# Kernel optimization log

Hardware: AMD Instinct MI355X
Metric: run time of the kernel (lower is better)

## Reference

```python
import jax, jax.numpy as jnp
import numpy as np

N_NODES = 100000
N_EDGES = 1250000
D = 64


def setup_inputs() -> dict:
    key = jax.random.key(0)
    k0, k1, k2, k3, k4 = jax.random.split(key, 5)
    feat = jax.random.normal(k0, (N_NODES, D), dtype=jnp.float32)
    src = jax.random.randint(k1, (N_EDGES,), 0, N_NODES)
    dst = jax.random.randint(k2, (N_EDGES,), 0, N_NODES)
    # GIN apply_func: Linear(D, D) -> ReLU -> Linear(D, D)
    scale = 1.0 / np.sqrt(D)
    W1 = jax.random.uniform(k3, (D, D), dtype=jnp.float32, minval=-scale, maxval=scale)
    b1 = jnp.zeros((D,), dtype=jnp.float32)
    W2 = jax.random.uniform(k4, (D, D), dtype=jnp.float32, minval=-scale, maxval=scale)
    b2 = jnp.zeros((D,), dtype=jnp.float32)
    eps = jnp.zeros((1,), dtype=jnp.float32)  # learnable eps, init 0
    return {"feat": feat, "W1": W1, "b1": b1, "W2": W2, "b2": b2,
            "eps": eps, "src": src, "dst": dst}


def reference(feat, W1, b1, W2, b2, eps, src, dst):
    # copy_u + sum reduce: gather source features per edge, scatter-add to dst
    msgs = feat[src]                                   # [E, D]
    neigh = jax.ops.segment_sum(msgs, dst, num_segments=feat.shape[0])  # [N, D]
    rst = (1.0 + eps) * feat + neigh                   # combine
    # apply_func (f_Theta): 2-layer MLP
    h = jax.nn.relu(rst @ W1 + b1)
    out = h @ W2 + b2
    return out
```

## Files before the change

kernel.cpp:

```cpp
#include <hip/hip_runtime.h>
#include <hip/hip_bf16.h>

#define N_NODES 100000
#define N_EDGES 1250000
#define DIM 64
#define NB 782
#define NCHUNK 512
#define CHUNK 2442
#define MAXE 4096

typedef __attribute__((ext_vector_type(8))) short short8;
typedef __attribute__((ext_vector_type(8))) __bf16 bf16x8;
typedef __attribute__((ext_vector_type(4))) float f32x4;

static __device__ __forceinline__ short f2bf(float f) {
    union { float f; unsigned u; } v; v.f = f;
    unsigned r = (v.u + 0x7fffu + ((v.u >> 16) & 1u)) >> 16;
    return (short)r;
}
static __device__ __forceinline__ float bflo(unsigned u) {
    union { unsigned u; float f; } v; v.u = u << 16; return v.f;
}
static __device__ __forceinline__ float bfhi(unsigned u) {
    union { unsigned u; float f; } v; v.u = u & 0xffff0000u; return v.f;
}
static __device__ __forceinline__ float bfs2f(short s) {
    union { unsigned u; float f; } v; v.u = ((unsigned)(unsigned short)s) << 16; return v.f;
}
static __device__ __forceinline__ int wave_scan(int v, int lane) {
#pragma unroll
    for (int off = 1; off < 64; off <<= 1) {
        int n = __shfl_up(v, off, 64);
        if (lane >= off) v += n;
    }
    return v;
}

__global__ __launch_bounds__(256) void prologue(const float* __restrict__ feat,
                                                short* __restrict__ featbf,
                                                const float* __restrict__ W1,
                                                const float* __restrict__ W2,
                                                short* __restrict__ wf,
                                                int basePrep) {
    int blk = blockIdx.x;
    if (blk < basePrep) {
        int i = (blk * 256 + threadIdx.x) * 8;
        float4 a = *(const float4*)(feat + i);
        float4 b = *(const float4*)(feat + i + 4);
        short8 t;
        t[0] = f2bf(a.x); t[1] = f2bf(a.y); t[2] = f2bf(a.z); t[3] = f2bf(a.w);
        t[4] = f2bf(b.x); t[5] = f2bf(b.y); t[6] = f2bf(b.z); t[7] = f2bf(b.w);
        *(short8*)(featbf + i) = t;
    } else {
        int idx = (blk - basePrep) * 256 + threadIdx.x;
        int layer = idx >> 12;
        int fi = idx & 4095;
        int fragidx = fi >> 9;
        int lane = (fi >> 3) & 63;
        int jj = fi & 7;
        int ct = fragidx >> 1, kt = fragidx & 1;
        int k = kt * 32 + (lane >> 4) * 8 + jj;
        int j = ct * 16 + (lane & 15);
        const float* W = layer ? W2 : W1;
        wf[idx] = f2bf(W[k * DIM + j]);
    }
}

__global__ __launch_bounds__(512) void partition3(const int* __restrict__ src,
                                                  const int* __restrict__ dst,
                                                  int* __restrict__ offs_gT,
                                                  int* __restrict__ edgebuf) {
    __shared__ int cnt[NB];
    __shared__ int lcur[NB];
    __shared__ int wsum[8];
    __shared__ int estage[CHUNK];

    int c = blockIdx.x;
    int t = threadIdx.x;
    int lane = t & 63, wv = t >> 6;
    int base = c * CHUNK;
    int end = base + CHUNK; if (end > N_EDGES) end = N_EDGES;

    for (int b = t; b < NB; b += 512) cnt[b] = 0;
    __syncthreads();
    for (int i = base + t; i < end; i += 512)
        atomicAdd(&cnt[dst[i] >> 7], 1);
    __syncthreads();

    int b0 = 2 * t, b1 = 2 * t + 1;
    int v0 = (b0 < NB) ? cnt[b0] : 0;
    int v1 = (b1 < NB) ? cnt[b1] : 0;
    int isc = wave_scan(v0 + v1, lane);
    if (lane == 63) wsum[wv] = isc;
    __syncthreads();
    if (wv == 0) {
        int s = (lane < 8) ? wsum[lane] : 0;
#pragma unroll
        for (int off = 1; off < 8; off <<= 1) {
            int n = __shfl_up(s, off, 64);
            if (lane >= off) s += n;
        }
        if (lane < 8) wsum[lane] = s;
    }
    __syncthreads();
    int ex = (wv ? wsum[wv - 1] : 0) + isc - (v0 + v1);
    if (b0 < NB) { lcur[b0] = ex;      offs_gT[(size_t)b0 * NCHUNK + c] = ex; }
    if (b1 < NB) { lcur[b1] = ex + v0; offs_gT[(size_t)b1 * NCHUNK + c] = ex + v0; }
    if (t == 511) offs_gT[(size_t)NB * NCHUNK + c] = wsum[7];
    __syncthreads();

    for (int i = base + t; i < end; i += 512) {
        int d = dst[i];
        int p = atomicAdd(&lcur[d >> 7], 1);
        estage[p] = src[i] | ((d & 127) << 17);
    }
    __syncthreads();

    int n = end - base;
    for (int i = t; i < n; i += 512) edgebuf[base + i] = estage[i];
}

template<int BF>
__global__ __launch_bounds__(512) void fused_gather_mlp(const int* __restrict__ offs_gT,
                                                        const int* __restrict__ edgebuf,
                                                        const void* __restrict__ featp,
                                                        const float* __restrict__ feat,
                                                        const short* __restrict__ wf,
                                                        const float* __restrict__ b1,
                                                        const float* __restrict__ b2,
                                                        const float* __restrict__ epsp,
                                                        float* __restrict__ out) {
    __shared__ union {
        struct { int ew[MAXE]; int es[MAXE]; } s;
        float tile[128][66];
    } u;
    __shared__ int cnt[128], offs[128], cur[128];
    __shared__ int slen[NCHUNK], dloc[NCHUNK];
    __shared__ int wsum[8];
    __shared__ int csum[2];

    int b = blockIdx.x;
    int node0 = b << 7;
    int tid = threadIdx.x;
    int lane = tid & 63, wv8 = tid >> 6;
    int c = tid & 15;
    int slot = tid >> 4;

    int s0 = offs_gT[(size_t)b * NCHUNK + tid];
    int myslen = offs_gT[(size_t)(b + 1) * NCHUNK + tid] - s0;
    int isc = wave_scan(myslen, lane);
    if (lane == 63) wsum[wv8] = isc;
    __syncthreads();
    if (wv8 == 0) {
        int s = (lane < 8) ? wsum[lane] : 0;
#pragma unroll
        for (int off = 1; off < 8; off <<= 1) {
            int n = __shfl_up(s, off, 64);
            if (lane >= off) s += n;
        }
        if (lane < 8) wsum[lane] = s;
    }
    __syncthreads();
    int incl = (wv8 ? wsum[wv8 - 1] : 0) + isc;
    dloc[tid] = incl - myslen;
    slen[tid] = myslen;
    int ec = wsum[7];
    __syncthreads();

    float acc[4][4];
#pragma unroll
    for (int g = 0; g < 4; ++g)
#pragma unroll
        for (int j = 0; j < 4; ++j) acc[g][j] = 0.f;

    int c0 = 0;
    while (c0 < NCHUNK) {
        int rbase = dloc[c0];
        int pred = (tid >= c0) && (dloc[tid] + slen[tid] - rbase <= MAXE);
        int nc = __syncthreads_count(pred);
        int c1 = c0 + nc;

        if (tid < 128) cnt[tid] = 0;
        if (tid >= c0 && tid < c1 && myslen > 0) {
            int d0 = dloc[tid] - rbase;
            const int* sp = edgebuf + (size_t)tid * CHUNK + s0;
            for (int i = 0; i < myslen; ++i) u.s.ew[d0 + i] = sp[i];
        }
        __syncthreads();

        int n = ((c1 < NCHUNK) ? dloc[c1] : ec) - rbase;

        for (int i = tid; i < n; i += 512)
            atomicAdd(&cnt[(u.s.ew[i] >> 17) & 127], 1);
        __syncthreads();

        int v_c = (tid < 128) ? cnt[tid] : 0;
        int s_c = 0;
        if (wv8 < 2) {
            s_c = wave_scan(v_c, lane);
            if (lane == 63) csum[wv8] = s_c;
        }
        __syncthreads();
        if (tid < 128) {
            int basec = (wv8 == 1) ? csum[0] : 0;
            int x = basec + s_c - v_c;
            offs[tid] = x;
            cur[tid] = x;
        }
        __syncthreads();

        for (int i = tid; i < n; i += 512) {
            int w = u.s.ew[i];
            int p = atomicAdd(&cur[(w >> 17) & 127], 1);
            u.s.es[p] = w & 0x1FFFF;
        }
        __syncthreads();

#pragma unroll
        for (int g = 0; g < 4; ++g) {
            int ld = g * 32 + slot;
            int e0 = offs[ld], e1 = e0 + cnt[ld];
            int i = e0;
            if (BF) {
                const uint2* fb = (const uint2*)featp;
                int nfull = (e1 - e0) & ~3;
                int efull = e0 + nfull;
                if (nfull) {
                    uint2 p0 = fb[u.s.es[i]     * 16 + c];
                    uint2 p1 = fb[u.s.es[i + 1] * 16 + c];
                    uint2 p2 = fb[u.s.es[i + 2] * 16 + c];
                    uint2 p3 = fb[u.s.es[i + 3] * 16 + c];
                    for (i = e0 + 4; i < efull; i += 4) {
                        uint2 q0 = fb[u.s.es[i]     * 16 + c];
                        uint2 q1 = fb[u.s.es[i + 1] * 16 + c];
                        uint2 q2 = fb[u.s.es[i + 2] * 16 + c];
                        uint2 q3 = fb[u.s.es[i + 3] * 16 + c];
                        acc[g][0] += bflo(p0.x) + bflo(p1.x) + bflo(p2.x) + bflo(p3.x);
                        acc[g][1] += bfhi(p0.x) + bfhi(p1.x) + bfhi(p2.x) + bfhi(p3.x);
                        acc[g][2] += bflo(p0.y) + bflo(p1.y) + bflo(p2.y) + bflo(p3.y);
                        acc[g][3] += bfhi(p0.y) + bfhi(p1.y) + bfhi(p2.y) + bfhi(p3.y);
                        p0 = q0; p1 = q1; p2 = q2; p3 = q3;
                    }
                    acc[g][0] += bflo(p0.x) + bflo(p1.x) + bflo(p2.x) + bflo(p3.x);
                    acc[g][1] += bfhi(p0.x) + bfhi(p1.x) + bfhi(p2.x) + bfhi(p3.x);
                    acc[g][2] += bflo(p0.y) + bflo(p1.y) + bflo(p2.y) + bflo(p3.y);
                    acc[g][3] += bfhi(p0.y) + bfhi(p1.y) + bfhi(p2.y) + bfhi(p3.y);
                }
                for (; i < e1; ++i) {
                    uint2 pa = fb[u.s.es[i] * 16 + c];
                    acc[g][0] += bflo(pa.x); acc[g][1] += bfhi(pa.x);
                    acc[g][2] += bflo(pa.y); acc[g][3] += bfhi(pa.y);
                }
            } else {
                const float4* ff = (const float4*)featp;
                int nfull = (e1 - e0) & ~1;
                int efull = e0 + nfull;
                if (nfull) {
                    float4 p0 = ff[u.s.es[i]     * 16 + c];
                    float4 p1 = ff[u.s.es[i + 1] * 16 + c];
                    for (i = e0 + 2; i < efull; i += 2) {
                        float4 q0 = ff[u.s.es[i]     * 16 + c];
                        float4 q1 = ff[u.s.es[i + 1] * 16 + c];
                        acc[g][0] += p0.x + p1.x; acc[g][1] += p0.y + p1.y;
                        acc[g][2] += p0.z + p1.z; acc[g][3] += p0.w + p1.w;
                        p0 = q0; p1 = q1;
                    }
                    acc[g][0] += p0.x + p1.x; acc[g][1] += p0.y + p1.y;
                    acc[g][2] += p0.z + p1.z; acc[g][3] += p0.w + p1.w;
                }
                for (; i < e1; ++i) {
                    float4 qa = ff[u.s.es[i] * 16 + c];
                    acc[g][0] += qa.x; acc[g][1] += qa.y;
                    acc[g][2] += qa.z; acc[g][3] += qa.w;
                }
            }
        }
        __syncthreads();
        c0 = c1;
    }

#pragma unroll
    for (int g = 0; g < 4; ++g) {
        int ld = g * 32 + slot;
#pragma unroll
        for (int j = 0; j < 4; ++j)
            u.tile[ld][c * 4 + j] = acc[g][j];
    }
    __syncthreads();

    int r = lane & 15, gg = lane >> 4;
    int lrow = wv8 * 16 + r;
    int node = node0 + lrow;
    bool valid = node < N_NODES;
    float epsv = 1.0f + epsp[0];

    const short8* w1f8 = (const short8*)(wf);
    const short8* w2f8 = (const short8*)(wf + 4096);

    short8 a[2];
#pragma unroll
    for (int kt = 0; kt < 2; ++kt) {
        float fv[8];
        if (BF) {
            short8 f8 = { 0,0,0,0,0,0,0,0 };
            if (valid) f8 = ((const short8*)featp)[node * 8 + kt * 4 + gg];
#pragma unroll
            for (int jj = 0; jj < 8; ++jj) fv[jj] = bfs2f(f8[jj]);
        } else {
            float4 f0 = { 0,0,0,0 }, f1 = { 0,0,0,0 };
            if (valid) {
                const float* fp = feat + (size_t)node * 64 + kt * 32 + gg * 8;
                f0 = *(const float4*)fp;
                f1 = *(const float4*)(fp + 4);
            }
            fv[0]=f0.x; fv[1]=f0.y; fv[2]=f0.z; fv[3]=f0.w;
            fv[4]=f1.x; fv[5]=f1.y; fv[6]=f1.z; fv[7]=f1.w;
        }
        const float2* tp = (const float2*)&u.tile[lrow][kt * 32 + gg * 8];
        float2 n0 = tp[0], n1 = tp[1], n2 = tp[2], n3 = tp[3];
        float rs[8] = { epsv * fv[0] + n0.x, epsv * fv[1] + n0.y,
                        epsv * fv[2] + n1.x, epsv * fv[3] + n1.y,
                        epsv * fv[4] + n2.x, epsv * fv[5] + n2.y,
                        epsv * fv[6] + n3.x, epsv * fv[7] + n3.y };
        short8 t;
#pragma unroll
        for (int jj = 0; jj < 8; ++jj) t[jj] = f2bf(rs[jj]);
        a[kt] = t;
    }
    __syncthreads();

    f32x4 acc1[4];
#pragma unroll
    for (int ct = 0; ct < 4; ++ct) {
        float bv = b1[ct * 16 + r];
        f32x4 cc = { bv, bv, bv, bv };
        cc = __builtin_amdgcn_mfma_f32_16x16x32_bf16(
                __builtin_bit_cast(bf16x8, a[0]),
                __builtin_bit_cast(bf16x8, w1f8[(ct * 2 + 0) * 64 + lane]),
                cc, 0, 0, 0);
        cc = __builtin_amdgcn_mfma_f32_16x16x32_bf16(
                __builtin_bit_cast(bf16x8, a[1]),
                __builtin_bit_cast(bf16x8, w1f8[(ct * 2 + 1) * 64 + lane]),
                cc, 0, 0, 0);
        acc1[ct] = cc;
    }

#pragma unroll
    for (int ct = 0; ct < 4; ++ct)
#pragma unroll
        for (int i = 0; i < 4; ++i)
            u.tile[wv8 * 16 + gg * 4 + i][ct * 16 + r] = fmaxf(acc1[ct][i], 0.0f);
    __syncthreads();

    short8 a2[2];
#pragma unroll
    for (int kt = 0; kt < 2; ++kt) {
        const float2* hp = (const float2*)&u.tile[wv8 * 16 + r][kt * 32 + gg * 8];
        float2 h0 = hp[0], h1 = hp[1], h2 = hp[2], h3 = hp[3];
        float hs[8] = { h0.x, h0.y, h1.x, h1.y, h2.x, h2.y, h3.x, h3.y };
        short8 t;
#pragma unroll
        for (int jj = 0; jj < 8; ++jj) t[jj] = f2bf(hs[jj]);
        a2[kt] = t;
    }

    f32x4 acc2[4];
#pragma unroll
    for (int ct = 0; ct < 4; ++ct) {
        float bv = b2[ct * 16 + r];
        f32x4 cc = { bv, bv, bv, bv };
        cc = __builtin_amdgcn_mfma_f32_16x16x32_bf16(
                __builtin_bit_cast(bf16x8, a2[0]),
                __builtin_bit_cast(bf16x8, w2f8[(ct * 2 + 0) * 64 + lane]),
                cc, 0, 0, 0);
        cc = __builtin_amdgcn_mfma_f32_16x16x32_bf16(
                __builtin_bit_cast(bf16x8, a2[1]),
                __builtin_bit_cast(bf16x8, w2f8[(ct * 2 + 1) * 64 + lane]),
                cc, 0, 0, 0);
        acc2[ct] = cc;
    }

#pragma unroll
    for (int ct = 0; ct < 4; ++ct)
#pragma unroll
        for (int i = 0; i < 4; ++i) {
            int nrow = node0 + wv8 * 16 + gg * 4 + i;
            if (nrow < N_NODES)
                out[(size_t)nrow * 64 + ct * 16 + r] = acc2[ct][i];
        }
}

__global__ __launch_bounds__(256) void scatter_edges(const float4* __restrict__ feat4,
                                                     const int* __restrict__ src,
                                                     const int* __restrict__ dst,
                                                     float* __restrict__ neigh) {
    int idx = blockIdx.x * 256 + threadIdx.x;
    int e = idx >> 4, c = idx & 15;
    int s = src[e], d = dst[e];
    float4 v = feat4[s * 16 + c];
    float* p = neigh + d * 64 + c * 4;
    unsafeAtomicAdd(p + 0, v.x);
    unsafeAtomicAdd(p + 1, v.y);
    unsafeAtomicAdd(p + 2, v.z);
    unsafeAtomicAdd(p + 3, v.w);
}

__global__ __launch_bounds__(256) void prep_w(const float* __restrict__ W1,
                                              const float* __restrict__ W2,
                                              short* __restrict__ wf) {
    int idx = blockIdx.x * 256 + threadIdx.x;
    int layer = idx >> 12;
    int fi = idx & 4095;
    int fragidx = fi >> 9;
    int lane = (fi >> 3) & 63;
    int jj = fi & 7;
    int ct = fragidx >> 1, kt = fragidx & 1;
    int k = kt * 32 + (lane >> 4) * 8 + jj;
    int j = ct * 16 + (lane & 15);
    const float* W = layer ? W2 : W1;
    wf[idx] = f2bf(W[k * DIM + j]);
}

__global__ __launch_bounds__(256) void gin_mlp(const float* __restrict__ feat,
                                               float* __restrict__ neigh_out,
                                               const short* __restrict__ wf,
                                               const float* __restrict__ b1,
                                               const float* __restrict__ b2,
                                               const float* __restrict__ epsp) {
    __shared__ float hbuf[4][16][66];
    int lane = threadIdx.x & 63;
    int wv = threadIdx.x >> 6;
    int r = lane & 15, g = lane >> 4;
    int row0 = blockIdx.x * 64 + wv * 16;
    int node = row0 + r;
    bool valid = node < N_NODES;
    float epsv = 1.0f + epsp[0];
    const short8* w1f8 = (const short8*)(wf);
    const short8* w2f8 = (const short8*)(wf + 4096);
    short8 a[2];
    if (valid) {
        const float* fp = feat + node * 64 + g * 8;
        const float* np_ = neigh_out + node * 64 + g * 8;
#pragma unroll
        for (int kt = 0; kt < 2; ++kt) {
            float4 f0 = *(const float4*)(fp + kt * 32);
            float4 f1 = *(const float4*)(fp + kt * 32 + 4);
            float4 n0 = *(const float4*)(np_ + kt * 32);
            float4 n1 = *(const float4*)(np_ + kt * 32 + 4);
            float rs[8] = { epsv * f0.x + n0.x, epsv * f0.y + n0.y,
                            epsv * f0.z + n0.z, epsv * f0.w + n0.w,
                            epsv * f1.x + n1.x, epsv * f1.y + n1.y,
                            epsv * f1.z + n1.z, epsv * f1.w + n1.w };
            short8 t;
#pragma unroll
            for (int jj = 0; jj < 8; ++jj) t[jj] = f2bf(rs[jj]);
            a[kt] = t;
        }
    } else {
        short8 z = { 0,0,0,0,0,0,0,0 };
        a[0] = z; a[1] = z;
    }
    f32x4 acc[4];
#pragma unroll
    for (int ct = 0; ct < 4; ++ct) {
        float bv = b1[ct * 16 + r];
        f32x4 c = { bv, bv, bv, bv };
        c = __builtin_amdgcn_mfma_f32_16x16x32_bf16(
                __builtin_bit_cast(bf16x8, a[0]),
                __builtin_bit_cast(bf16x8, w1f8[(ct * 2 + 0) * 64 + lane]), c, 0, 0, 0);
        c = __builtin_amdgcn_mfma_f32_16x16x32_bf16(
                __builtin_bit_cast(bf16x8, a[1]),
                __builtin_bit_cast(bf16x8, w1f8[(ct * 2 + 1) * 64 + lane]), c, 0, 0, 0);
        acc[ct] = c;
    }
#pragma unroll
    for (int ct = 0; ct < 4; ++ct)
#pragma unroll
        for (int i = 0; i < 4; ++i)
            hbuf[wv][g * 4 + i][ct * 16 + r] = fmaxf(acc[ct][i], 0.0f);
    __syncthreads();
    short8 a2[2];
#pragma unroll
    for (int kt = 0; kt < 2; ++kt) {
        const float2* hp = (const float2*)&hbuf[wv][r][kt * 32 + g * 8];
        float2 h0 = hp[0], h1 = hp[1], h2 = hp[2], h3 = hp[3];
        float hs[8] = { h0.x, h0.y, h1.x, h1.y, h2.x, h2.y, h3.x, h3.y };
        short8 t;
#pragma unroll
        for (int jj = 0; jj < 8; ++jj) t[jj] = f2bf(hs[jj]);
        a2[kt] = t;
    }
    f32x4 acc2[4];
#pragma unroll
    for (int ct = 0; ct < 4; ++ct) {
        float bv = b2[ct * 16 + r];
        f32x4 c = { bv, bv, bv, bv };
        c = __builtin_amdgcn_mfma_f32_16x16x32_bf16(
                __builtin_bit_cast(bf16x8, a2[0]),
                __builtin_bit_cast(bf16x8, w2f8[(ct * 2 + 0) * 64 + lane]), c, 0, 0, 0);
        c = __builtin_amdgcn_mfma_f32_16x16x32_bf16(
                __builtin_bit_cast(bf16x8, a2[1]),
                __builtin_bit_cast(bf16x8, w2f8[(ct * 2 + 1) * 64 + lane]), c, 0, 0, 0);
        acc2[ct] = c;
    }
#pragma unroll
    for (int ct = 0; ct < 4; ++ct)
#pragma unroll
        for (int i = 0; i < 4; ++i) {
            int nrow = row0 + g * 4 + i;
            if (nrow < N_NODES)
                neigh_out[nrow * 64 + ct * 16 + r] = acc2[ct][i];
        }
}

extern "C" void kernel_launch(void* const* d_in, const int* in_sizes, int n_in,
                              void* d_out, int out_size, void* d_ws, size_t ws_size,
                              hipStream_t stream) {
    const float* feat = (const float*)d_in[0];
    const float* W1   = (const float*)d_in[1];
    const float* b1   = (const float*)d_in[2];
    const float* W2   = (const float*)d_in[3];
    const float* b2   = (const float*)d_in[4];
    const float* eps  = (const float*)d_in[5];
    const int*   src  = (const int*)d_in[6];
    const int*   dst  = (const int*)d_in[7];
    float* out = (float*)d_out;

    char* ws = (char*)d_ws;
    short* wf = (short*)ws;

    const size_t featbf_bytes = (size_t)N_NODES * DIM * 2;
    const size_t offs_bytes   = (size_t)(NB + 1) * NCHUNK * 4;
    const size_t edge_bytes   = (size_t)NCHUNK * CHUNK * 4;
    const size_t need_mid  = 16384 + offs_bytes + edge_bytes;
    const size_t need_full = need_mid + featbf_bytes;

    if (ws_size >= need_mid) {
        char* p = ws + 16384;
        short* featbf = nullptr;
        if (ws_size >= need_full) { featbf = (short*)p; p += featbf_bytes; }
        int* offs_gT = (int*)p;            p += offs_bytes;
        int* edgebuf = (int*)p;

        int basePrep = featbf ? 3125 : 0;
        prologue<<<basePrep + 32, 256, 0, stream>>>(feat, featbf, W1, W2, wf, basePrep);

        partition3<<<NCHUNK, 512, 0, stream>>>(src, dst, offs_gT, edgebuf);

        if (featbf)
            fused_gather_mlp<1><<<NB, 512, 0, stream>>>(
                offs_gT, edgebuf, featbf, feat, wf, b1, b2, eps, out);
        else
            fused_gather_mlp<0><<<NB, 512, 0, stream>>>(
                offs_gT, edgebuf, feat, feat, wf, b1, b2, eps, out);
    } else {
        prep_w<<<32, 256, 0, stream>>>(W1, W2, wf);
        hipMemsetAsync(d_out, 0, (size_t)N_NODES * DIM * sizeof(float), stream);
        scatter_edges<<<(N_EDGES * 16) / 256, 256, 0, stream>>>(
            (const float4*)feat, src, dst, out);
        gin_mlp<<<(N_NODES + 63) / 64, 256, 0, stream>>>(feat, out, wf, b1, b2, eps);
    }
}
```

Before: 73.06 us.

## Split gather into feature-quarter blocks with quarter-major bf16 layout and separate MLP kernel

Reorders the bf16 feature copy into four 16-column quarter planes so each gather block touches only one 32-byte slice per source node. The gather kernel is launched with four times as many blocks, one per quarter of each destination tile, and writes fp32 neighbour sums to a workspace buffer. A separate MLP kernel then reads them back. The aim is more parallelism and a smaller per-block cache footprint. The cost is that every block repeats the edge bucketing and sort work, plus an extra fp32 round trip through global memory and one more launch. The fp32 fallback path that applied when the workspace was smaller is also removed.

New measurement: 86.50 us. +18.4%, slower.

```diff
diff --git a/kernel.cpp b/kernel.cpp
--- a/kernel.cpp
+++ b/kernel.cpp
@@ -37,7 +37,7 @@
 }
 
 __global__ __launch_bounds__(256) void prologue(const float* __restrict__ feat,
-                                                short* __restrict__ featbf,
+                                                short* __restrict__ featq,
                                                 const float* __restrict__ W1,
                                                 const float* __restrict__ W2,
                                                 short* __restrict__ wf,
@@ -50,7 +50,10 @@
         short8 t;
         t[0] = f2bf(a.x); t[1] = f2bf(a.y); t[2] = f2bf(a.z); t[3] = f2bf(a.w);
         t[4] = f2bf(b.x); t[5] = f2bf(b.y); t[6] = f2bf(b.z); t[7] = f2bf(b.w);
-        *(short8*)(featbf + i) = t;
+        int node = i >> 6;
+        int d0 = i & 63;
+        int q = d0 >> 4, dq = d0 & 15;
+        *(short8*)(featq + ((size_t)(q * N_NODES + node) * 16 + dq)) = t;
     } else {
         int idx = (blk - basePrep) * 256 + threadIdx.x;
         int layer = idx >> 12;
@@ -120,31 +123,26 @@
     for (int i = t; i < n; i += 512) edgebuf[base + i] = estage[i];
 }
 
-template<int BF>
-__global__ __launch_bounds__(512) void fused_gather_mlp(const int* __restrict__ offs_gT,
-                                                        const int* __restrict__ edgebuf,
-                                                        const void* __restrict__ featp,
-                                                        const float* __restrict__ feat,
-                                                        const short* __restrict__ wf,
-                                                        const float* __restrict__ b1,
-                                                        const float* __restrict__ b2,
-                                                        const float* __restrict__ epsp,
-                                                        float* __restrict__ out) {
-    __shared__ union {
-        struct { int ew[MAXE]; int es[MAXE]; } s;
-        float tile[128][66];
-    } u;
+__global__ __launch_bounds__(512) void gather_q(const int* __restrict__ offs_gT,
+                                                const int* __restrict__ edgebuf,
+                                                const short* __restrict__ featq,
+                                                float4* __restrict__ nq4) {
+    __shared__ int ew[MAXE];
+    __shared__ int es[MAXE];
     __shared__ int cnt[128], offs[128], cur[128];
     __shared__ int slen[NCHUNK], dloc[NCHUNK];
     __shared__ int wsum[8];
     __shared__ int csum[2];
 
-    int b = blockIdx.x;
+    int blk = blockIdx.x;
+    int b = blk >> 2;
+    int q = blk & 3;
     int node0 = b << 7;
+    int qbase = q * N_NODES;
     int tid = threadIdx.x;
     int lane = tid & 63, wv8 = tid >> 6;
-    int c = tid & 15;
-    int slot = tid >> 4;
+    int c2 = tid & 3;
+    int slot = tid >> 2;
 
     int s0 = offs_gT[(size_t)b * NCHUNK + tid];
     int myslen = offs_gT[(size_t)(b + 1) * NCHUNK + tid] - s0;
@@ -167,11 +165,8 @@
     int ec = wsum[7];
     __syncthreads();
 
-    float acc[4][4];
-#pragma unroll
-    for (int g = 0; g < 4; ++g)
-#pragma unroll
-        for (int j = 0; j < 4; ++j) acc[g][j] = 0.f;
+    float acc0 = 0.f, acc1 = 0.f, acc2 = 0.f, acc3 = 0.f;
+    const uint2* fb = (const uint2*)featq;
 
     int c0 = 0;
     while (c0 < NCHUNK) {
@@ -184,14 +179,14 @@
         if (tid >= c0 && tid < c1 && myslen > 0) {
             int d0 = dloc[tid] - rbase;
             const int* sp = edgebuf + (size_t)tid * CHUNK + s0;
-            for (int i = 0; i < myslen; ++i) u.s.ew[d0 + i] = sp[i];
+            for (int i = 0; i < myslen; ++i) ew[d0 + i] = sp[i];
         }
         __syncthreads();
 
         int n = ((c1 < NCHUNK) ? dloc[c1] : ec) - rbase;
 
         for (int i = tid; i < n; i += 512)
-            atomicAdd(&cnt[(u.s.ew[i] >> 17) & 127], 1);
+            atomicAdd(&cnt[(ew[i] >> 17) & 127], 1);
         __syncthreads();
 
         int v_c = (tid < 128) ? cnt[tid] : 0;
@@ -210,87 +205,56 @@
         __syncthreads();
 
         for (int i = tid; i < n; i += 512) {
-            int w = u.s.ew[i];
+            int w = ew[i];
             int p = atomicAdd(&cur[(w >> 17) & 127], 1);
-            u.s.es[p] = w & 0x1FFFF;
+            es[p] = w & 0x1FFFF;
         }
         __syncthreads();
 
-#pragma unroll
-        for (int g = 0; g < 4; ++g) {
-            int ld = g * 32 + slot;
-            int e0 = offs[ld], e1 = e0 + cnt[ld];
+        {
+            int e0 = offs[slot], e1 = e0 + cnt[slot];
             int i = e0;
-            if (BF) {
-                const uint2* fb = (const uint2*)featp;
-                int nfull = (e1 - e0) & ~3;
-                int efull = e0 + nfull;
-                if (nfull) {
-                    uint2 p0 = fb[u.s.es[i]     * 16 + c];
-                    uint2 p1 = fb[u.s.es[i + 1] * 16 + c];
-                    uint2 p2 = fb[u.s.es[i + 2] * 16 + c];
-                    uint2 p3 = fb[u.s.es[i + 3] * 16 + c];
-                    for (i = e0 + 4; i < efull; i += 4) {
-                        uint2 q0 = fb[u.s.es[i]     * 16 + c];
-                        uint2 q1 = fb[u.s.es[i + 1] * 16 + c];
-                        uint2 q2 = fb[u.s.es[i + 2] * 16 + c];
-                        uint2 q3 = fb[u.s.es[i + 3] * 16 + c];
-                        acc[g][0] += bflo(p0.x) + bflo(p1.x) + bflo(p2.x) + bflo(p3.x);
-                        acc[g][1] += bfhi(p0.x) + bfhi(p1.x) + bfhi(p2.x) + bfhi(p3.x);
-                        acc[g][2] += bflo(p0.y) + bflo(p1.y) + bflo(p2.y) + bflo(p3.y);
-                        acc[g][3] += bfhi(p0.y) + bfhi(p1.y) + bfhi(p2.y) + bfhi(p3.y);
-                        p0 = q0; p1 = q1; p2 = q2; p3 = q3;
-                    }
-                    acc[g][0] += bflo(p0.x) + bflo(p1.x) + bflo(p2.x) + bflo(p3.x);
-                    acc[g][1] += bfhi(p0.x) + bfhi(p1.x) + bfhi(p2.x) + bfhi(p3.x);
-                    acc[g][2] += bflo(p0.y) + bflo(p1.y) + bflo(p2.y) + bflo(p3.y);
-                    acc[g][3] += bfhi(p0.y) + bfhi(p1.y) + bfhi(p2.y) + bfhi(p3.y);
-                }
-                for (; i < e1; ++i) {
-                    uint2 pa = fb[u.s.es[i] * 16 + c];
-                    acc[g][0] += bflo(pa.x); acc[g][1] += bfhi(pa.x);
-                    acc[g][2] += bflo(pa.y); acc[g][3] += bfhi(pa.y);
-                }
-            } else {
-                const float4* ff = (const float4*)featp;
-                int nfull = (e1 - e0) & ~1;
-                int efull = e0 + nfull;
-                if (nfull) {
-                    float4 p0 = ff[u.s.es[i]     * 16 + c];
-                    float4 p1 = ff[u.s.es[i + 1] * 16 + c];
-                    for (i = e0 + 2; i < efull; i += 2) {
-                        float4 q0 = ff[u.s.es[i]     * 16 + c];
-                        float4 q1 = ff[u.s.es[i + 1] * 16 + c];
-                        acc[g][0] += p0.x + p1.x; acc[g][1] += p0.y + p1.y;
-                        acc[g][2] += p0.z + p1.z; acc[g][3] += p0.w + p1.w;
-                        p0 = q0; p1 = q1;
-                    }
-                    acc[g][0] += p0.x + p1.x; acc[g][1] += p0.y + p1.y;
-                    acc[g][2] += p0.z + p1.z; acc[g][3] += p0.w + p1.w;
-                }
-                for (; i < e1; ++i) {
-                    float4 qa = ff[u.s.es[i] * 16 + c];
-                    acc[g][0] += qa.x; acc[g][1] += qa.y;
-                    acc[g][2] += qa.z; acc[g][3] += qa.w;
-                }
+            for (; i + 3 < e1; i += 4) {
+                int sa = es[i], sb = es[i + 1], sc_ = es[i + 2], sd = es[i + 3];
+                uint2 p0 = fb[(qbase + sa) * 4 + c2];
+                uint2 p1 = fb[(qbase + sb) * 4 + c2];
+                uint2 p2 = fb[(qbase + sc_) * 4 + c2];
+                uint2 p3 = fb[(qbase + sd) * 4 + c2];
+                acc0 += bflo(p0.x) + bflo(p1.x) + bflo(p2.x) + bflo(p3.x);
+                acc1 += bfhi(p0.x) + bfhi(p1.x) + bfhi(p2.x) + bfhi(p3.x);
+                acc2 += bflo(p0.y) + bflo(p1.y) + bflo(p2.y) + bflo(p3.y);
+                acc3 += bfhi(p0.y) + bfhi(p1.y) + bfhi(p2.y) + bfhi(p3.y);
+            }
+            for (; i < e1; ++i) {
+                uint2 pa = fb[(qbase + es[i]) * 4 + c2];
+                acc0 += bflo(pa.x); acc1 += bfhi(pa.x);
+                acc2 += bflo(pa.y); acc3 += bfhi(pa.y);
             }
         }
         __syncthreads();
         c0 = c1;
     }
 
-#pragma unroll
-    for (int g = 0; g < 4; ++g) {
-        int ld = g * 32 + slot;
-#pragma unroll
-        for (int j = 0; j < 4; ++j)
-            u.tile[ld][c * 4 + j] = acc[g][j];
-    }
-    __syncthreads();
-
-    int r = lane & 15, gg = lane >> 4;
-    int lrow = wv8 * 16 + r;
-    int node = node0 + lrow;
+    int node = node0 + slot;
+    if (node < N_NODES) {
+        float4 v = { acc0, acc1, acc2, acc3 };
+        nq4[(size_t)(qbase + node) * 4 + c2] = v;
+    }
+}
+
+__global__ __launch_bounds__(256) void mlp_q(const short* __restrict__ featq,
+                                             const float4* __restrict__ nq4,
+                                             const short* __restrict__ wf,
+                                             const float* __restrict__ b1,
+                                             const float* __restrict__ b2,
+                                             const float* __restrict__ epsp,
+                                             float* __restrict__ out) {
+    __shared__ float hbuf[4][16][66];
+    int lane = threadIdx.x & 63;
+    int wv = threadIdx.x >> 6;
+    int r = lane & 15, g = lane >> 4;
+    int row0 = blockIdx.x * 64 + wv * 16;
+    int node = row0 + r;
     bool valid = node < N_NODES;
     float epsv = 1.0f + epsp[0];
 
@@ -300,34 +264,28 @@
     short8 a[2];
 #pragma unroll
     for (int kt = 0; kt < 2; ++kt) {
+        int d0 = kt * 32 + g * 8;
+        int q = d0 >> 4, dq = d0 & 15;
         float fv[8];
-        if (BF) {
-            short8 f8 = { 0,0,0,0,0,0,0,0 };
-            if (valid) f8 = ((const short8*)featp)[node * 8 + kt * 4 + gg];
-#pragma unroll
-            for (int jj = 0; jj < 8; ++jj) fv[jj] = bfs2f(f8[jj]);
-        } else {
-            float4 f0 = { 0,0,0,0 }, f1 = { 0,0,0,0 };
-            if (valid) {
-                const float* fp = feat + (size_t)node * 64 + kt * 32 + gg * 8;
-                f0 = *(const float4*)fp;
-                f1 = *(const float4*)(fp + 4);
-            }
-            fv[0]=f0.x; fv[1]=f0.y; fv[2]=f0.z; fv[3]=f0.w;
-            fv[4]=f1.x; fv[5]=f1.y; fv[6]=f1.z; fv[7]=f1.w;
-        }
-        const float2* tp = (const float2*)&u.tile[lrow][kt * 32 + gg * 8];
-        float2 n0 = tp[0], n1 = tp[1], n2 = tp[2], n3 = tp[3];
+        float4 n0 = { 0,0,0,0 }, n1 = { 0,0,0,0 };
+        short8 f8 = { 0,0,0,0,0,0,0,0 };
+        if (valid) {
+            int rowb = q * N_NODES + node;
+            f8 = ((const short8*)featq)[rowb * 2 + (dq >> 3)];
+            n0 = nq4[(size_t)rowb * 4 + (dq >> 2)];
+            n1 = nq4[(size_t)rowb * 4 + (dq >> 2) + 1];
+        }
+#pragma unroll
+        for (int jj = 0; jj < 8; ++jj) fv[jj] = bfs2f(f8[jj]);
         float rs[8] = { epsv * fv[0] + n0.x, epsv * fv[1] + n0.y,
-                        epsv * fv[2] + n1.x, epsv * fv[3] + n1.y,
-                        epsv * fv[4] + n2.x, epsv * fv[5] + n2.y,
-                        epsv * fv[6] + n3.x, epsv * fv[7] + n3.y };
+                        epsv * fv[2] + n0.z, epsv * fv[3] + n0.w,
+                        epsv * fv[4] + n1.x, epsv * fv[5] + n1.y,
+                        epsv * fv[6] + n1.z, epsv * fv[7] + n1.w };
         short8 t;
 #pragma unroll
         for (int jj = 0; jj < 8; ++jj) t[jj] = f2bf(rs[jj]);
         a[kt] = t;
     }
-    __syncthreads();
 
     f32x4 acc1[4];
 #pragma unroll
@@ -349,13 +307,13 @@
     for (int ct = 0; ct < 4; ++ct)
 #pragma unroll
         for (int i = 0; i < 4; ++i)
-            u.tile[wv8 * 16 + gg * 4 + i][ct * 16 + r] = fmaxf(acc1[ct][i], 0.0f);
+            hbuf[wv][g * 4 + i][ct * 16 + r] = fmaxf(acc1[ct][i], 0.0f);
     __syncthreads();
 
     short8 a2[2];
 #pragma unroll
     for (int kt = 0; kt < 2; ++kt) {
-        const float2* hp = (const float2*)&u.tile[wv8 * 16 + r][kt * 32 + gg * 8];
+        const float2* hp = (const float2*)&hbuf[wv][r][kt * 32 + g * 8];
         float2 h0 = hp[0], h1 = hp[1], h2 = hp[2], h3 = hp[3];
         float hs[8] = { h0.x, h0.y, h1.x, h1.y, h2.x, h2.y, h3.x, h3.y };
         short8 t;
@@ -384,7 +342,7 @@
     for (int ct = 0; ct < 4; ++ct)
 #pragma unroll
         for (int i = 0; i < 4; ++i) {
-            int nrow = node0 + wv8 * 16 + gg * 4 + i;
+            int nrow = row0 + g * 4 + i;
             if (nrow < N_NODES)
                 out[(size_t)nrow * 64 + ct * 16 + r] = acc2[ct][i];
         }
@@ -529,30 +487,28 @@
     char* ws = (char*)d_ws;
     short* wf = (short*)ws;
 
-    const size_t featbf_bytes = (size_t)N_NODES * DIM * 2;
+    const size_t featq_bytes  = (size_t)N_NODES * DIM * 2;
     const size_t offs_bytes   = (size_t)(NB + 1) * NCHUNK * 4;
     const size_t edge_bytes   = (size_t)NCHUNK * CHUNK * 4;
-    const size_t need_mid  = 16384 + offs_bytes + edge_bytes;
-    const size_t need_full = need_mid + featbf_bytes;
-
-    if (ws_size >= need_mid) {
+    const size_t neighq_bytes = (size_t)N_NODES * DIM * 4;
+    const size_t need_full = 16384 + featq_bytes + offs_bytes + edge_bytes + neighq_bytes;
+
+    if (ws_size >= need_full) {
         char* p = ws + 16384;
-        short* featbf = nullptr;
-        if (ws_size >= need_full) { featbf = (short*)p; p += featbf_bytes; }
-        int* offs_gT = (int*)p;            p += offs_bytes;
-        int* edgebuf = (int*)p;
-
-        int basePrep = featbf ? 3125 : 0;
-        prologue<<<basePrep + 32, 256, 0, stream>>>(feat, featbf, W1, W2, wf, basePrep);
+        short* featq   = (short*)p;        p += featq_bytes;
+        int* offs_gT   = (int*)p;          p += offs_bytes;
+        int* edgebuf   = (int*)p;          p += edge_bytes;
+        float4* neighq = (float4*)p;
+
+        int basePrep = 3125;
+        prologue<<<basePrep + 32, 256, 0, stream>>>(feat, featq, W1, W2, wf, basePrep);
 
         partition3<<<NCHUNK, 512, 0, stream>>>(src, dst, offs_gT, edgebuf);
 
-        if (featbf)
-            fused_gather_mlp<1><<<NB, 512, 0, stream>>>(
-                offs_gT, edgebuf, featbf, feat, wf, b1, b2, eps, out);
-        else
-            fused_gather_mlp<0><<<NB, 512, 0, stream>>>(
-                offs_gT, edgebuf, feat, feat, wf, b1, b2, eps, out);
+        gather_q<<<NB * 4, 512, 0, stream>>>(offs_gT, edgebuf, featq, neighq);
+
+        mlp_q<<<(N_NODES + 63) / 64, 256, 0, stream>>>(
+            featq, neighq, wf, b1, b2, eps, out);
     } else {
         prep_w<<<32, 256, 0, stream>>>(W1, W2, wf);
         hipMemsetAsync(d_out, 0, (size_t)N_NODES * DIM * sizeof(float), stream);
```
